# Kernel tuning notes

Hardware: AMD Instinct MI355X
Metric: run time of the kernel (lower is better)

Reference implementation:

```python
import jax, jax.numpy as jnp
import numpy as np


def _conv1d_same(seq, w, b):
    # seq: (N, 1, C), w: (1, 1, K) odd K, bias (1,). SAME padding, stride 1.
    k = w.shape[-1]
    p = (k - 1) // 2
    out = jax.lax.conv_general_dilated(
        seq, w, window_strides=(1,), padding=[(p, p)],
        dimension_numbers=("NCH", "OIH", "NCH"))
    return out + b[None, :, None]


def setup_inputs() -> dict:
    key = jax.random.key(0)
    k1, k2, k3 = jax.random.split(key, 3)
    N, C, H, W = 32, 512, 32, 32
    x = jax.random.normal(k1, (N, C, H, W), dtype=jnp.float32)
    wq = jax.random.normal(k2, (1, 1, 5), dtype=jnp.float32) * 0.2
    bq = jax.random.normal(k3, (1,), dtype=jnp.float32) * 0.1
    return {"x": x, "wq": wq, "bq": bq}


def reference(x, wq, bq):
    N, C, H, W = x.shape
    # Global average pool over spatial dims -> (N, 1, C)
    gap = jnp.mean(x, axis=(2, 3)).reshape(N, 1, C)
    # NOTE: original module applies conv_q to BOTH query and key (conv_k unused)
    query = jax.nn.sigmoid(_conv1d_same(gap, wq, bq))          # (N, 1, C)
    key_t = jnp.transpose(query, (0, 2, 1))                    # (N, C, 1)
    # Outer product key @ query -> (N, C, C), softmax over flattened C*C
    qk = jnp.einsum("nci,nij->ncj", key_t, query)              # (N, C, C)
    qk = jax.nn.softmax(qk.reshape(N, C * C), axis=-1).reshape(N, C, C)
    # value: (N, H*W, C)
    value = jnp.transpose(x, (0, 2, 3, 1)).reshape(N, H * W, C)
    att = jnp.einsum("npc,ncd->npd", value, qk)                # (N, HW, C)
    att = jnp.transpose(att, (0, 2, 1)).reshape(N, C, H, W)
    return x * att
```

## Files before the change

### kernel.cpp

```cpp
#include <hip/hip_runtime.h>
#include <hip/hip_cooperative_groups.h>
#include <math.h>

namespace cg = cooperative_groups;

#define NB 32
#define CC 512
#define HW 1024
#define NJ 10

__device__ __forceinline__ float wave_reduce(float s) {
#pragma unroll
  for (int off = 32; off; off >>= 1) s += __shfl_down(s, off, 64);
  return s;
}

__global__ __launch_bounds__(512, 4) void k_onepass(
    const float* __restrict__ x, const float* __restrict__ wq,
    const float* __restrict__ bq, float* __restrict__ out,
    float* __restrict__ gpart) {
  int b = blockIdx.x;
  int n = b >> 4;
  int t = threadIdx.x;
  int cg = t >> 4, pg = t & 15;
  int wv = t >> 6, lane = t & 63;

  __shared__ float gs[CC];
  __shared__ float qs[CC];
  __shared__ float wred[8][NJ];
  __shared__ float4 sred[8][16][NJ + 1];
  __shared__ float4 sfin[16][NJ + 1];
  __shared__ float invZ_sh;

  const float cj[NJ] = {1.f, 1.f, 0.5f, 1.f / 6.f, 1.f / 24.f, 1.f / 120.f,
                        1.f / 720.f, 1.f / 5040.f, 1.f / 40320.f, 1.f / 362880.f};

  float4 xv[16];
  const float4* x4 = (const float4*)x;
  size_t base = (size_t)(n * CC + cg * 16) * 256 + (size_t)(b & 15) * 16 + pg;
#pragma unroll
  for (int i = 0; i < 16; ++i) xv[i] = x4[base + (size_t)i * 256];

  {
    float ps[16];
#pragma unroll
    for (int i = 0; i < 16; ++i) {
      float4 v = xv[i];
      ps[i] = v.x + v.y + v.z + v.w;
    }
#pragma unroll
    for (int off = 1; off < 16; off <<= 1) {
#pragma unroll
      for (int i = 0; i < 16; ++i) ps[i] += __shfl_xor(ps[i], off, 64);
    }
    if (pg == 0) {
#pragma unroll
      for (int i = 0; i < 16; ++i) gs[cg * 16 + i] = ps[i];
    }
  }
  __syncthreads();
  if (t < 128) ((float4*)&gpart[(size_t)b * CC])[t] = ((const float4*)gs)[t];

  cg::this_grid().sync();

  {
    int c = t;
    float g = 0.f;
#pragma unroll
    for (int pb = 0; pb < 16; ++pb) g += gpart[(size_t)(n * 16 + pb) * CC + c];
    gs[c] = g * (1.0f / 1024.0f);
  }
  __syncthreads();
  {
    int c = t;
    float z = bq[0];
#pragma unroll
    for (int k = 0; k < 5; ++k) {
      int idx = c + k - 2;
      float gv = (idx >= 0 && idx < CC) ? gs[idx] : 0.f;
      z = fmaf(gv, wq[k], z);
    }
    float qv = 1.f / (1.f + expf(-z));
    qs[c] = qv;
    float pj[NJ];
    float pw = 1.f;
#pragma unroll
    for (int j = 0; j < NJ; ++j) { pj[j] = pw; pw *= qv; }
#pragma unroll
    for (int j = 0; j < NJ; ++j) pj[j] = wave_reduce(pj[j]);
    if (lane == 0) {
#pragma unroll
      for (int j = 0; j < NJ; ++j) wred[wv][j] = pj[j];
    }
  }
  __syncthreads();
  if (t == 0) {
    float Z = 0.f;
#pragma unroll
    for (int j = 0; j < NJ; ++j) {
      float P = 0.f;
#pragma unroll
      for (int w8 = 0; w8 < 8; ++w8) P += wred[w8][j];
      Z = fmaf(cj[j] * P, P, Z);
    }
    invZ_sh = 1.f / Z;
  }

#pragma unroll
  for (int half = 0; half < 2; ++half) {
    float4 acc[5];
#pragma unroll
    for (int j = 0; j < 5; ++j) acc[j] = make_float4(0.f, 0.f, 0.f, 0.f);
#pragma unroll
    for (int i = 0; i < 16; ++i) {
      float qc = qs[cg * 16 + i];
      float4 v = xv[i];
      float w;
      if (half == 0) w = 1.f;
      else { float q2 = qc * qc; w = q2 * q2 * qc; }
#pragma unroll
      for (int j = 0; j < 5; ++j) {
        acc[j].x = fmaf(w, v.x, acc[j].x);
        acc[j].y = fmaf(w, v.y, acc[j].y);
        acc[j].z = fmaf(w, v.z, acc[j].z);
        acc[j].w = fmaf(w, v.w, acc[j].w);
        w *= qc;
      }
    }
#pragma unroll
    for (int j = 0; j < 5; ++j) {
      acc[j].x += __shfl_xor(acc[j].x, 16, 64);
      acc[j].y += __shfl_xor(acc[j].y, 16, 64);
      acc[j].z += __shfl_xor(acc[j].z, 16, 64);
      acc[j].w += __shfl_xor(acc[j].w, 16, 64);
      acc[j].x += __shfl_xor(acc[j].x, 32, 64);
      acc[j].y += __shfl_xor(acc[j].y, 32, 64);
      acc[j].z += __shfl_xor(acc[j].z, 32, 64);
      acc[j].w += __shfl_xor(acc[j].w, 32, 64);
    }
    if (lane < 16) {
#pragma unroll
      for (int j = 0; j < 5; ++j) sred[wv][lane][half * 5 + j] = acc[j];
    }
  }
  __syncthreads();
  if (t < 160) {
    int pp = t / NJ, j = t - pp * NJ;
    float4 a = make_float4(0.f, 0.f, 0.f, 0.f);
#pragma unroll
    for (int w8 = 0; w8 < 8; ++w8) {
      float4 v = sred[w8][pp][j];
      a.x += v.x; a.y += v.y; a.z += v.z; a.w += v.w;
    }
    float sc = cj[j] * invZ_sh;
    a.x *= sc; a.y *= sc; a.z *= sc; a.w *= sc;
    sfin[pp][j] = a;
  }
  __syncthreads();

  float4 sj[NJ];
#pragma unroll
  for (int j = 0; j < NJ; ++j) sj[j] = sfin[pg][j];
  float4* o4 = (float4*)out;
#pragma unroll
  for (int i = 0; i < 16; ++i) {
    float qd = qs[cg * 16 + i];
    float w = 1.f;
    float4 att = make_float4(0.f, 0.f, 0.f, 0.f);
#pragma unroll
    for (int j = 0; j < NJ; ++j) {
      att.x = fmaf(w, sj[j].x, att.x);
      att.y = fmaf(w, sj[j].y, att.y);
      att.z = fmaf(w, sj[j].z, att.z);
      att.w = fmaf(w, sj[j].w, att.w);
      w *= qd;
    }
    float4 xvv = xv[i];
    float4 o;
    o.x = xvv.x * att.x; o.y = xvv.y * att.y;
    o.z = xvv.z * att.z; o.w = xvv.w * att.w;
    o4[base + (size_t)i * 256] = o;
  }
}

__global__ __launch_bounds__(256) void k_gap(const float* __restrict__ x,
                                             float* __restrict__ gap) {
  int wv = threadIdx.x >> 6, lane = threadIdx.x & 63;
  int r0 = blockIdx.x * 16;
#pragma unroll
  for (int it = 0; it < 4; ++it) {
    int row = r0 + wv * 4 + it;
    const float4* xp = (const float4*)x + (size_t)row * 256;
    float s = 0.f;
#pragma unroll
    for (int k = 0; k < 4; ++k) {
      float4 v = xp[lane + 64 * k];
      s += v.x + v.y + v.z + v.w;
    }
    s = wave_reduce(s);
    if (lane == 0) gap[row] = s * (1.0f / 1024.0f);
  }
}

__global__ __launch_bounds__(512) void k_fused(const float* __restrict__ x,
                                               const float* __restrict__ gap,
                                               const float* __restrict__ wq,
                                               const float* __restrict__ bq,
                                               float* __restrict__ out) {
  int n = blockIdx.x >> 4, pblk = blockIdx.x & 15;
  int t = threadIdx.x;
  int cg = t >> 4, pg = t & 15;
  int wv = t >> 6, lane = t & 63;

  __shared__ float qs[CC];
  __shared__ float wred[8][NJ];
  __shared__ float4 sred[8][16][NJ + 1];
  __shared__ float4 sfin[16][NJ + 1];
  __shared__ float invZ_sh;

  const float cj[NJ] = {1.f, 1.f, 0.5f, 1.f / 6.f, 1.f / 24.f, 1.f / 120.f,
                        1.f / 720.f, 1.f / 5040.f, 1.f / 40320.f, 1.f / 362880.f};

  float4 xv[16];
  const float4* x4 = (const float4*)x;
  size_t base = (size_t)(n * CC + cg * 16) * 256 + (size_t)pblk * 16 + pg;
#pragma unroll
  for (int i = 0; i < 16; ++i) xv[i] = x4[base + (size_t)i * 256];

  {
    int c = t;
    const float* g = gap + n * CC;
    float z = bq[0];
#pragma unroll
    for (int k = 0; k < 5; ++k) {
      int idx = c + k - 2;
      float gv = (idx >= 0 && idx < CC) ? g[idx] : 0.f;
      z = fmaf(gv, wq[k], z);
    }
    float qv = 1.f / (1.f + expf(-z));
    qs[c] = qv;
    float pj[NJ];
    float pw = 1.f;
#pragma unroll
    for (int j = 0; j < NJ; ++j) { pj[j] = pw; pw *= qv; }
#pragma unroll
    for (int j = 0; j < NJ; ++j) pj[j] = wave_reduce(pj[j]);
    if (lane == 0) {
#pragma unroll
      for (int j = 0; j < NJ; ++j) wred[wv][j] = pj[j];
    }
  }
  __syncthreads();
  if (t == 0) {
    float Z = 0.f;
#pragma unroll
    for (int j = 0; j < NJ; ++j) {
      float P = 0.f;
#pragma unroll
      for (int w8 = 0; w8 < 8; ++w8) P += wred[w8][j];
      Z = fmaf(cj[j] * P, P, Z);
    }
    invZ_sh = 1.f / Z;
  }

  float4 acc[NJ];
#pragma unroll
  for (int j = 0; j < NJ; ++j) acc[j] = make_float4(0.f, 0.f, 0.f, 0.f);
#pragma unroll
  for (int i = 0; i < 16; ++i) {
    float qc = qs[cg * 16 + i];
    float4 v = xv[i];
    float w = 1.f;
#pragma unroll
    for (int j = 0; j < NJ; ++j) {
      acc[j].x = fmaf(w, v.x, acc[j].x);
      acc[j].y = fmaf(w, v.y, acc[j].y);
      acc[j].z = fmaf(w, v.z, acc[j].z);
      acc[j].w = fmaf(w, v.w, acc[j].w);
      w *= qc;
    }
  }
#pragma unroll
  for (int j = 0; j < NJ; ++j) {
    acc[j].x += __shfl_xor(acc[j].x, 16, 64);
    acc[j].y += __shfl_xor(acc[j].y, 16, 64);
    acc[j].z += __shfl_xor(acc[j].z, 16, 64);
    acc[j].w += __shfl_xor(acc[j].w, 16, 64);
    acc[j].x += __shfl_xor(acc[j].x, 32, 64);
    acc[j].y += __shfl_xor(acc[j].y, 32, 64);
    acc[j].z += __shfl_xor(acc[j].z, 32, 64);
    acc[j].w += __shfl_xor(acc[j].w, 32, 64);
  }
  if (lane < 16) {
#pragma unroll
    for (int j = 0; j < NJ; ++j) sred[wv][lane][j] = acc[j];
  }
  __syncthreads();
  if (t < 160) {
    int pp = t / NJ, j = t - pp * NJ;
    float4 a = make_float4(0.f, 0.f, 0.f, 0.f);
#pragma unroll
    for (int w8 = 0; w8 < 8; ++w8) {
      float4 v = sred[w8][pp][j];
      a.x += v.x; a.y += v.y; a.z += v.z; a.w += v.w;
    }
    float sc = cj[j] * invZ_sh;
    a.x *= sc; a.y *= sc; a.z *= sc; a.w *= sc;
    sfin[pp][j] = a;
  }
  __syncthreads();

  float4 sj[NJ];
#pragma unroll
  for (int j = 0; j < NJ; ++j) sj[j] = sfin[pg][j];
  float4* o4 = (float4*)out;
#pragma unroll
  for (int i = 0; i < 16; ++i) {
    float qd = qs[cg * 16 + i];
    float w = 1.f;
    float4 att = make_float4(0.f, 0.f, 0.f, 0.f);
#pragma unroll
    for (int j = 0; j < NJ; ++j) {
      att.x = fmaf(w, sj[j].x, att.x);
      att.y = fmaf(w, sj[j].y, att.y);
      att.z = fmaf(w, sj[j].z, att.z);
      att.w = fmaf(w, sj[j].w, att.w);
      w *= qd;
    }
    float4 xvv = xv[i];
    float4 o;
    o.x = xvv.x * att.x; o.y = xvv.y * att.y;
    o.z = xvv.z * att.z; o.w = xvv.w * att.w;
    o4[base + (size_t)i * 256] = o;
  }
}

extern "C" void kernel_launch(void* const* d_in, const int* in_sizes, int n_in,
                              void* d_out, int out_size, void* d_ws, size_t ws_size,
                              hipStream_t stream) {
  const float* x  = (const float*)d_in[0];
  const float* wq = (const float*)d_in[1];
  const float* bq = (const float*)d_in[2];
  float* out = (float*)d_out;
  float* gpart = (float*)d_ws;

  int maxB = 0;
  (void)hipOccupancyMaxActiveBlocksPerMultiprocessor(&maxB, (const void*)k_onepass,
                                                     512, 0);
  if (maxB >= 2) {
    void* args[] = {(void*)&x, (void*)&wq, (void*)&bq, (void*)&out, (void*)&gpart};
    hipLaunchCooperativeKernel((const void*)k_onepass, dim3(NB * 16), dim3(512),
                               args, 0, stream);
  } else {
    float* gap = gpart;
    k_gap<<<NB * CC / 16, 256, 0, stream>>>(x, gap);
    k_fused<<<NB * 16, 512, 0, stream>>>(x, gap, wq, bq, out);
  }
}
```

Before: 132.9 us.

## Halve grid to one block per CU, use atomic-counter grid barrier

Cuts the cooperative grid from 512 to 256 blocks, so each block holds 32 channels × 32 float4 positions in registers. The cooperative-groups grid sync is replaced by a hand-rolled atomic counter barrier with sleep polling, and the counter is reset by a memset before each launch. The two-half power accumulation becomes a single 10-term pass with fewer shuffles. The price is a much higher register footprint (xv[32] plus acc[10] float4) and possible spills, plus an extra memset call, in exchange for cheaper synchronisation and reduction.

After: 132.8 us. About the same (-0.1%).

```diff
diff --git a/kernel.cpp b/kernel.cpp
--- a/kernel.cpp
+++ b/kernel.cpp
@@ -1,12 +1,8 @@
 #include <hip/hip_runtime.h>
-#include <hip/hip_cooperative_groups.h>
 #include <math.h>
-
-namespace cg = cooperative_groups;
 
 #define NB 32
 #define CC 512
-#define HW 1024
 #define NJ 10
 
 __device__ __forceinline__ float wave_reduce(float s) {
@@ -15,59 +11,67 @@
   return s;
 }
 
-__global__ __launch_bounds__(512, 4) void k_onepass(
+__global__ __launch_bounds__(512, 2) void k_onepass(
     const float* __restrict__ x, const float* __restrict__ wq,
     const float* __restrict__ bq, float* __restrict__ out,
-    float* __restrict__ gpart) {
+    float* __restrict__ gpart, unsigned* __restrict__ cnt) {
   int b = blockIdx.x;
-  int n = b >> 4;
+  int n = b >> 3, pb = b & 7;
   int t = threadIdx.x;
-  int cg = t >> 4, pg = t & 15;
+  int cg = t >> 5, pg = t & 31;
   int wv = t >> 6, lane = t & 63;
 
   __shared__ float gs[CC];
   __shared__ float qs[CC];
   __shared__ float wred[8][NJ];
-  __shared__ float4 sred[8][16][NJ + 1];
-  __shared__ float4 sfin[16][NJ + 1];
+  __shared__ float4 sred[8][32][NJ + 1];
+  __shared__ float4 sfin[32][NJ + 1];
   __shared__ float invZ_sh;
 
   const float cj[NJ] = {1.f, 1.f, 0.5f, 1.f / 6.f, 1.f / 24.f, 1.f / 120.f,
                         1.f / 720.f, 1.f / 5040.f, 1.f / 40320.f, 1.f / 362880.f};
 
-  float4 xv[16];
+  float4 xv[32];
   const float4* x4 = (const float4*)x;
-  size_t base = (size_t)(n * CC + cg * 16) * 256 + (size_t)(b & 15) * 16 + pg;
-#pragma unroll
-  for (int i = 0; i < 16; ++i) xv[i] = x4[base + (size_t)i * 256];
+  size_t base = (size_t)(n * CC + cg * 32) * 256 + (size_t)pb * 32 + pg;
+#pragma unroll
+  for (int i = 0; i < 32; ++i) xv[i] = x4[base + (size_t)i * 256];
 
   {
-    float ps[16];
-#pragma unroll
-    for (int i = 0; i < 16; ++i) {
+    float ps[32];
+#pragma unroll
+    for (int i = 0; i < 32; ++i) {
       float4 v = xv[i];
       ps[i] = v.x + v.y + v.z + v.w;
     }
 #pragma unroll
-    for (int off = 1; off < 16; off <<= 1) {
-#pragma unroll
-      for (int i = 0; i < 16; ++i) ps[i] += __shfl_xor(ps[i], off, 64);
+    for (int off = 1; off < 32; off <<= 1) {
+#pragma unroll
+      for (int i = 0; i < 32; ++i) ps[i] += __shfl_xor(ps[i], off, 64);
     }
     if (pg == 0) {
-#pragma unroll
-      for (int i = 0; i < 16; ++i) gs[cg * 16 + i] = ps[i];
-    }
-  }
-  __syncthreads();
-  if (t < 128) ((float4*)&gpart[(size_t)b * CC])[t] = ((const float4*)gs)[t];
-
-  cg::this_grid().sync();
+      float* gp = gpart + (size_t)b * CC + cg * 32;
+#pragma unroll
+      for (int i = 0; i < 32; ++i) gp[i] = ps[i];
+    }
+  }
+
+  __syncthreads();
+  if (t == 0) {
+    __threadfence();
+    atomicAdd(cnt, 1u);
+    while (__hip_atomic_load(cnt, __ATOMIC_ACQUIRE, __HIP_MEMORY_SCOPE_AGENT) <
+           256u) {
+      __builtin_amdgcn_s_sleep(2);
+    }
+  }
+  __syncthreads();
 
   {
     int c = t;
     float g = 0.f;
 #pragma unroll
-    for (int pb = 0; pb < 16; ++pb) g += gpart[(size_t)(n * 16 + pb) * CC + c];
+    for (int k = 0; k < 8; ++k) g += gpart[(size_t)(n * 8 + k) * CC + c];
     gs[c] = g * (1.0f / 1024.0f);
   }
   __syncthreads();
@@ -106,45 +110,36 @@
     invZ_sh = 1.f / Z;
   }
 
-#pragma unroll
-  for (int half = 0; half < 2; ++half) {
-    float4 acc[5];
-#pragma unroll
-    for (int j = 0; j < 5; ++j) acc[j] = make_float4(0.f, 0.f, 0.f, 0.f);
-#pragma unroll
-    for (int i = 0; i < 16; ++i) {
-      float qc = qs[cg * 16 + i];
-      float4 v = xv[i];
-      float w;
-      if (half == 0) w = 1.f;
-      else { float q2 = qc * qc; w = q2 * q2 * qc; }
-#pragma unroll
-      for (int j = 0; j < 5; ++j) {
-        acc[j].x = fmaf(w, v.x, acc[j].x);
-        acc[j].y = fmaf(w, v.y, acc[j].y);
-        acc[j].z = fmaf(w, v.z, acc[j].z);
-        acc[j].w = fmaf(w, v.w, acc[j].w);
-        w *= qc;
-      }
-    }
-#pragma unroll
-    for (int j = 0; j < 5; ++j) {
-      acc[j].x += __shfl_xor(acc[j].x, 16, 64);
-      acc[j].y += __shfl_xor(acc[j].y, 16, 64);
-      acc[j].z += __shfl_xor(acc[j].z, 16, 64);
-      acc[j].w += __shfl_xor(acc[j].w, 16, 64);
-      acc[j].x += __shfl_xor(acc[j].x, 32, 64);
-      acc[j].y += __shfl_xor(acc[j].y, 32, 64);
-      acc[j].z += __shfl_xor(acc[j].z, 32, 64);
-      acc[j].w += __shfl_xor(acc[j].w, 32, 64);
-    }
-    if (lane < 16) {
-#pragma unroll
-      for (int j = 0; j < 5; ++j) sred[wv][lane][half * 5 + j] = acc[j];
-    }
-  }
-  __syncthreads();
-  if (t < 160) {
+  float4 acc[NJ];
+#pragma unroll
+  for (int j = 0; j < NJ; ++j) acc[j] = make_float4(0.f, 0.f, 0.f, 0.f);
+#pragma unroll
+  for (int i = 0; i < 32; ++i) {
+    float qc = qs[cg * 32 + i];
+    float4 v = xv[i];
+    float w = 1.f;
+#pragma unroll
+    for (int j = 0; j < NJ; ++j) {
+      acc[j].x = fmaf(w, v.x, acc[j].x);
+      acc[j].y = fmaf(w, v.y, acc[j].y);
+      acc[j].z = fmaf(w, v.z, acc[j].z);
+      acc[j].w = fmaf(w, v.w, acc[j].w);
+      w *= qc;
+    }
+  }
+#pragma unroll
+  for (int j = 0; j < NJ; ++j) {
+    acc[j].x += __shfl_xor(acc[j].x, 32, 64);
+    acc[j].y += __shfl_xor(acc[j].y, 32, 64);
+    acc[j].z += __shfl_xor(acc[j].z, 32, 64);
+    acc[j].w += __shfl_xor(acc[j].w, 32, 64);
+  }
+  if (lane < 32) {
+#pragma unroll
+    for (int j = 0; j < NJ; ++j) sred[wv][lane][j] = acc[j];
+  }
+  __syncthreads();
+  if (t < 320) {
     int pp = t / NJ, j = t - pp * NJ;
     float4 a = make_float4(0.f, 0.f, 0.f, 0.f);
 #pragma unroll
@@ -163,8 +158,8 @@
   for (int j = 0; j < NJ; ++j) sj[j] = sfin[pg][j];
   float4* o4 = (float4*)out;
 #pragma unroll
-  for (int i = 0; i < 16; ++i) {
-    float qd = qs[cg * 16 + i];
+  for (int i = 0; i < 32; ++i) {
+    float qd = qs[cg * 32 + i];
     float w = 1.f;
     float4 att = make_float4(0.f, 0.f, 0.f, 0.f);
 #pragma unroll
@@ -342,16 +337,23 @@
   const float* wq = (const float*)d_in[1];
   const float* bq = (const float*)d_in[2];
   float* out = (float*)d_out;
-  float* gpart = (float*)d_ws;
+  char* ws = (char*)d_ws;
+
+  unsigned* cnt = (unsigned*)ws;
+  float* gpart  = (float*)(ws + 256);
 
   int maxB = 0;
   (void)hipOccupancyMaxActiveBlocksPerMultiprocessor(&maxB, (const void*)k_onepass,
                                                      512, 0);
-  if (maxB >= 2) {
-    void* args[] = {(void*)&x, (void*)&wq, (void*)&bq, (void*)&out, (void*)&gpart};
-    hipLaunchCooperativeKernel((const void*)k_onepass, dim3(NB * 16), dim3(512),
-                               args, 0, stream);
-  } else {
+  hipError_t err = hipErrorUnknown;
+  if (maxB >= 1) {
+    hipMemsetAsync(ws, 0, 256, stream);
+    void* args[] = {(void*)&x, (void*)&wq, (void*)&bq, (void*)&out,
+                    (void*)&gpart, (void*)&cnt};
+    err = hipLaunchCooperativeKernel((const void*)k_onepass, dim3(256), dim3(512),
+                                     args, 0, stream);
+  }
+  if (err != hipSuccess) {
     float* gap = gpart;
     k_gap<<<NB * CC / 16, 256, 0, stream>>>(x, gap);
     k_fused<<<NB * 16, 512, 0, stream>>>(x, gap, wq, bq, out);
```
